# Kernel optimization log

Hardware: AMD Instinct MI355X
Metric: run time of the kernel (lower is better)

The kernel has to match this reference:

```python
import jax, jax.numpy as jnp
import numpy as np

K = 3  # == stride, neighbors per token


def setup_inputs() -> dict:
    key = jax.random.key(0)
    k1, k2, k3 = jax.random.split(key, 3)
    x = jax.random.normal(k1, (16, 64, 2048), dtype=jnp.float32)        # (B, C, T)
    W = jax.random.normal(k2, (64, 64, K), dtype=jnp.float32) * 0.05     # (O, I, K) conv1d weight
    b = jax.random.normal(k3, (64,), dtype=jnp.float32) * 0.05           # (O,) conv1d bias
    return {"x": x, "W": W, "b": b}


def reference(x, W, b):
    B, C, T = x.shape
    # pairwise squared euclidean distances over the channel dim: (B, T, T)
    nsq = jnp.sum(x * x, axis=1)                       # (B, T)
    dot = jnp.einsum('bct,bcs->bts', x, x)             # (B, T, T)
    dist = jnp.maximum(nsq[:, :, None] + nsq[:, None, :] - 2.0 * dot, 0.0)
    # K nearest neighbors (smallest distance -> top_k of negated dist)
    _, idx = jax.lax.top_k(-dist, K)                   # (B, T, K) int32 indices
    # gather neighbor features: prime[b, c, i*K + k] = x[b, c, idx[b, i, k]]
    idx_flat = idx.reshape(B, 1, T * K)
    prime = jnp.take_along_axis(x, jnp.broadcast_to(idx_flat, (B, C, T * K)), axis=2)
    # Conv1d with kernel_size=K, stride=K, padding=0 -> output length T
    out = jax.lax.conv_general_dilated(
        prime, W, window_strides=(K,), padding='VALID',
        dimension_numbers=('NCH', 'OIH', 'NCH'))
    return out + b[None, :, None]
```

## Files before the change

### kernel.cpp

```cpp
#include <hip/hip_runtime.h>

#define B_ 16
#define C_ 64
#define T_ 2048
#define O_ 64
#define KNN 3
#define HSPLIT 4
#define JCH (T_ / HSPLIT)
#define NJS (JCH / 32)

typedef short short8   __attribute__((ext_vector_type(8)));
typedef float f32x4    __attribute__((ext_vector_type(4)));
typedef unsigned short ushortx4 __attribute__((ext_vector_type(4)));

#define XT_OFF 0
#define XS_OFF (XT_OFF + B_ * T_ * C_)
#define NSQ_OFF (XS_OFF + B_ * T_ * C_)
#define WT_OFF (NSQ_OFF + B_ * T_)
#define CAND_OFF (WT_OFF + 192 * O_)

__device__ inline ushort bf16_rne(float f) {
    union { float f; unsigned u; } cv; cv.f = f;
    unsigned u = cv.u;
    u += 0x7FFF + ((u >> 16) & 1);
    return (ushort)(u >> 16);
}
__device__ inline float bf16_val(ushort h) {
    union { unsigned u; float f; } cv; cv.u = ((unsigned)h) << 16; return cv.f;
}

__global__ __launch_bounds__(256) void prep_kernel(const float* __restrict__ x,
                                                   const float* __restrict__ W,
                                                   float* __restrict__ ws) {
    float*  xT  = ws + XT_OFF;
    ushort* xs  = (ushort*)(ws + XS_OFF);
    float*  nsq = ws + NSQ_OFF;
    float*  Wt  = ws + WT_OFF;
    int blk = blockIdx.x;
    int tid = threadIdx.x;
    if (blk < B_ * (T_ / 64)) {
        int b  = blk / (T_ / 64);
        int t0 = (blk % (T_ / 64)) * 64;
        __shared__ float tl[64 * 65];
        #pragma unroll
        for (int r = 0; r < 4; ++r) {
            int c  = r * 16 + (tid >> 4);
            int t4 = (tid & 15) * 4;
            float4 v = *(const float4*)(x + (size_t)(b * C_ + c) * T_ + t0 + t4);
            tl[c * 65 + t4 + 0] = v.x;
            tl[c * 65 + t4 + 1] = v.y;
            tl[c * 65 + t4 + 2] = v.z;
            tl[c * 65 + t4 + 3] = v.w;
        }
        __syncthreads();
        #pragma unroll
        for (int r = 0; r < 4; ++r) {
            int t  = r * 16 + (tid >> 4);
            int c0 = (tid & 15) * 4;
            float v0 = tl[(c0 + 0) * 65 + t];
            float v1 = tl[(c0 + 1) * 65 + t];
            float v2 = tl[(c0 + 2) * 65 + t];
            float v3 = tl[(c0 + 3) * 65 + t];
            size_t rowg = (size_t)(b * T_ + t0 + t);
            float4 xv; xv.x = v0; xv.y = v1; xv.z = v2; xv.w = v3;
            *(float4*)(xT + rowg * 64 + c0) = xv;
            ushort h0 = bf16_rne(v0), h1 = bf16_rne(v1);
            ushort h2 = bf16_rne(v2), h3 = bf16_rne(v3);
            ushortx4 hv; hv[0] = h0; hv[1] = h1; hv[2] = h2; hv[3] = h3;
            ushortx4 lv;
            lv[0] = bf16_rne(v0 - bf16_val(h0));
            lv[1] = bf16_rne(v1 - bf16_val(h1));
            lv[2] = bf16_rne(v2 - bf16_val(h2));
            lv[3] = bf16_rne(v3 - bf16_val(h3));
            *(ushortx4*)(xs + rowg * 128 + c0)      = hv;
            *(ushortx4*)(xs + rowg * 128 + 64 + c0) = lv;
        }
        if (tid < 64) {
            float s = 0.f;
            #pragma unroll
            for (int c = 0; c < 64; ++c) { float v = tl[c * 65 + tid]; s = fmaf(v, v, s); }
            nsq[b * T_ + t0 + tid] = s;
        }
    } else {
        int e = (blk - B_ * (T_ / 64)) * 256 + tid;
        if (e < O_ * C_ * KNN) {
            int o = e / (C_ * KNN);
            int c = (e / KNN) % C_;
            int k = e % KNN;
            Wt[(k * 64 + c) * O_ + o] = W[e];
        }
    }
}

__global__ __launch_bounds__(256, 4) void knn_mfma_kernel(const ushort* __restrict__ xs,
                                                          const float* __restrict__ nsq,
                                                          ushort* __restrict__ cand) {
    __shared__ __align__(16) ushort jbuf[4][32 * 128];
    __shared__ float nsqs[JCH];

    int bid = blockIdx.x;
    int b   = (bid & 7) + 8 * (bid >> 9);
    int h   = (bid >> 3) & 3;
    int m   = (bid >> 5) & 15;
    int i0  = m * 128;
    int tid = threadIdx.x;
    int w   = tid >> 6, l = tid & 63, lr = l & 15, lq = l >> 4;
    const ushort* xsb = xs + (size_t)b * T_ * 128;
    int jBase = h * JCH;

    if (tid < JCH / 4)
        ((float4*)nsqs)[tid] = ((const float4*)(nsq + b * T_ + jBase))[tid];

    short8 bA0, bA1, bA4, bA5, bB0, bB1, bB4, bB5;
    {
        const ushort* ia = xsb + (size_t)(i0 + w * 32 + lr) * 128 + lq * 8;
        bA0 = *(const short8*)(ia + 0);  bA1 = *(const short8*)(ia + 32);
        bA4 = *(const short8*)(ia + 64); bA5 = *(const short8*)(ia + 96);
        const ushort* ib2 = ia + 16 * 128;
        bB0 = *(const short8*)(ib2 + 0);  bB1 = *(const short8*)(ib2 + 32);
        bB4 = *(const short8*)(ib2 + 64); bB5 = *(const short8*)(ib2 + 96);
    }
    float niA = nsq[b * T_ + i0 + w * 32 + lr] + 4.0f;
    float niB = nsq[b * T_ + i0 + w * 32 + 16 + lr] + 4.0f;

    const float INF = __builtin_inff();
    float kA0 = INF, kA1 = INF, kA2 = INF, kA3 = INF;
    float kB0 = INF, kB1 = INF, kB2 = INF, kB3 = INF;

    int cSw = lr ^ (w * 4 + lq);
    #define ISSUE_DMA(jsv, bufv) {                                               \
        _Pragma("unroll")                                                        \
        for (int p = 0; p < 2; ++p) {                                            \
            int rloc = p * 16 + w * 4 + lq;                                      \
            const ushort* gp = xsb + (size_t)(jBase + (jsv) * 32 + rloc) * 128 + cSw * 8; \
            __builtin_amdgcn_global_load_lds(                                    \
                (const __attribute__((address_space(1))) void*)gp,               \
                (__attribute__((address_space(3))) void*)(jbuf[bufv] + (p * 16 + w * 4) * 128), \
                16, 0, 0);                                                       \
        } }

    asm volatile("s_waitcnt lgkmcnt(0)" ::: "memory");

    ISSUE_DMA(0, 0);
    ISSUE_DMA(1, 1);
    ISSUE_DMA(2, 2);

    #pragma unroll 1
    for (int js = 0; js < NJS; ++js) {
        if (js <= NJS - 3)      asm volatile("s_waitcnt vmcnt(4)" ::: "memory");
        else if (js == NJS - 2) asm volatile("s_waitcnt vmcnt(2)" ::: "memory");
        else                    asm volatile("s_waitcnt vmcnt(0)" ::: "memory");
        __builtin_amdgcn_s_barrier();
        asm volatile("" ::: "memory");
        __builtin_amdgcn_sched_barrier(0);
        if (js + 3 < NJS) ISSUE_DMA(js + 3, (js + 3) & 3);
        const char* jb8 = (const char*)jbuf[js & 3];
        #pragma unroll
        for (int tile = 0; tile < 2; ++tile) {
            const char* rowp = jb8 + (tile * 16 + lr) * 256;
            short8 ah0 = *(const short8*)(rowp + ((( 0 + lq) ^ lr) << 4));
            short8 ah1 = *(const short8*)(rowp + ((( 4 + lq) ^ lr) << 4));
            short8 al0 = *(const short8*)(rowp + ((( 8 + lq) ^ lr) << 4));
            short8 al1 = *(const short8*)(rowp + (((12 + lq) ^ lr) << 4));
            f32x4 accA = {0.f, 0.f, 0.f, 0.f};
            f32x4 accB = {0.f, 0.f, 0.f, 0.f};
            accA = __builtin_amdgcn_mfma_f32_16x16x32_bf16(ah0, bA0, accA, 0, 0, 0);
            accB = __builtin_amdgcn_mfma_f32_16x16x32_bf16(ah0, bB0, accB, 0, 0, 0);
            accA = __builtin_amdgcn_mfma_f32_16x16x32_bf16(ah1, bA1, accA, 0, 0, 0);
            accB = __builtin_amdgcn_mfma_f32_16x16x32_bf16(ah1, bB1, accB, 0, 0, 0);
            accA = __builtin_amdgcn_mfma_f32_16x16x32_bf16(al0, bA0, accA, 0, 0, 0);
            accB = __builtin_amdgcn_mfma_f32_16x16x32_bf16(al0, bB0, accB, 0, 0, 0);
            accA = __builtin_amdgcn_mfma_f32_16x16x32_bf16(al1, bA1, accA, 0, 0, 0);
            accB = __builtin_amdgcn_mfma_f32_16x16x32_bf16(al1, bB1, accB, 0, 0, 0);
            accA = __builtin_amdgcn_mfma_f32_16x16x32_bf16(ah0, bA4, accA, 0, 0, 0);
            accB = __builtin_amdgcn_mfma_f32_16x16x32_bf16(ah0, bB4, accB, 0, 0, 0);
            accA = __builtin_amdgcn_mfma_f32_16x16x32_bf16(ah1, bA5, accA, 0, 0, 0);
            accB = __builtin_amdgcn_mfma_f32_16x16x32_bf16(ah1, bB5, accB, 0, 0, 0);
            float4 nv = *(const float4*)(nsqs + js * 32 + tile * 16 + lq * 4);
            int idb = ((js * 2 + tile) << 2) | (lq << 8);
            #define INS(K0, K1, K2, K3, sv, idv) {                                  \
                unsigned uu = (__float_as_uint(sv) & 0xFFFFFC00u) | (unsigned)(idv); \
                float kf = __uint_as_float(uu);                                      \
                float n0 = fminf(K0, kf);                                            \
                float n1 = __builtin_amdgcn_fmed3f(K0, K1, kf);                      \
                float n2 = __builtin_amdgcn_fmed3f(K1, K2, kf);                      \
                float n3 = __builtin_amdgcn_fmed3f(K2, K3, kf);                      \
                K0 = n0; K1 = n1; K2 = n2; K3 = n3; }
            {
                float s0 = fmaf(-2.f, accA[0], nv.x + niA); INS(kA0, kA1, kA2, kA3, s0, idb + 0);
                float s1 = fmaf(-2.f, accA[1], nv.y + niA); INS(kA0, kA1, kA2, kA3, s1, idb + 1);
                float s2 = fmaf(-2.f, accA[2], nv.z + niA); INS(kA0, kA1, kA2, kA3, s2, idb + 2);
                float s3 = fmaf(-2.f, accA[3], nv.w + niA); INS(kA0, kA1, kA2, kA3, s3, idb + 3);
            }
            {
                float s0 = fmaf(-2.f, accB[0], nv.x + niB); INS(kB0, kB1, kB2, kB3, s0, idb + 0);
                float s1 = fmaf(-2.f, accB[1], nv.y + niB); INS(kB0, kB1, kB2, kB3, s1, idb + 1);
                float s2 = fmaf(-2.f, accB[2], nv.z + niB); INS(kB0, kB1, kB2, kB3, s2, idb + 2);
                float s3 = fmaf(-2.f, accB[3], nv.w + niB); INS(kB0, kB1, kB2, kB3, s3, idb + 3);
            }
            #undef INS
        }
    }

    __syncthreads();
    float* fbuf = (float*)jbuf;
    {
        float* pa = fbuf + (w * 32 + lr) * 16 + lq * 4;
        pa[0] = kA0; pa[1] = kA1; pa[2] = kA2; pa[3] = kA3;
        float* pb = fbuf + (w * 32 + 16 + lr) * 16 + lq * 4;
        pb[0] = kB0; pb[1] = kB1; pb[2] = kB2; pb[3] = kB3;
    }
    __syncthreads();
    if (l < 32) {
        int rloc = w * 32 + l;
        const float* pr = fbuf + rloc * 16;
        float m0 = INF, m1 = INF, m2 = INF, m3 = INF;
        #pragma unroll
        for (int q2 = 0; q2 < 16; ++q2) {
            float kf = pr[q2];
            float n0 = fminf(m0, kf);
            float n1 = __builtin_amdgcn_fmed3f(m0, m1, kf);
            float n2 = __builtin_amdgcn_fmed3f(m1, m2, kf);
            float n3 = __builtin_amdgcn_fmed3f(m2, m3, kf);
            m0 = n0; m1 = n1; m2 = n2; m3 = n3;
        }
        ushortx4 cv;
        #define DEC(mf, slot) { unsigned u = __float_as_uint(mf) & 1023u;            \
            cv[slot] = (ushort)(jBase + (((u >> 2) & 63u) << 4) + ((u >> 8) << 2) + (u & 3)); }
        DEC(m0, 0); DEC(m1, 1); DEC(m2, 2); DEC(m3, 3);
        #undef DEC
        int row = b * T_ + i0 + rloc;
        *(ushortx4*)(cand + (size_t)row * 16 + h * 4) = cv;
    }
}

__global__ __launch_bounds__(256, 4) void conv_fused_kernel(const float* __restrict__ ws,
                                                            const float* __restrict__ bias,
                                                            float* __restrict__ out) {
    const float*  xT   = ws + XT_OFF;
    const float*  nsq  = ws + NSQ_OFF;
    const float*  Wt   = ws + WT_OFF;
    const ushort* cand = (const ushort*)(ws + CAND_OFF);

    __shared__ float g_s[192 * 32];
    __shared__ int   jsel3[32 * 3];

    float* sref = g_s;
    int*   jref = (int*)(g_s + 32 * 17);
    float* q_s  = g_s + 1152;

    int bid = blockIdx.x;
    int bb  = (bid & 7) + 8 * (bid >> 9);
    int i0  = ((bid >> 3) & 63) * 32;
    int tid = threadIdx.x;
    int w = tid >> 6, l = tid & 63;
    int bT = bb * T_;

    {
        int row = tid >> 3;
        int c8  = tid & 7;
        const float4* src = (const float4*)(xT + (size_t)(bT + i0 + row) * 64 + c8 * 8);
        float4 v0 = src[0], v1 = src[1];
        *(float4*)(q_s + row * 68 + c8 * 8)     = v0;
        *(float4*)(q_s + row * 68 + c8 * 8 + 4) = v1;
    }

    const float INF = __builtin_inff();
    int cd  = l >> 2;
    int c16 = l & 3;
    int rbase = i0 + w * 8;
    int jtA[8];
    #pragma unroll
    for (int rr = 0; rr < 8; ++rr)
        jtA[rr] = cand[(size_t)(bT + rbase + rr) * 16 + cd];
    float nsqj[8];
    #pragma unroll
    for (int rr = 0; rr < 8; ++rr)
        nsqj[rr] = nsq[bT + jtA[rr]];

    #pragma unroll
    for (int rp = 0; rp < 2; ++rp) {
        float4 bv0[4], bv1[4], bv2[4], bv3[4];
        #pragma unroll
        for (int r4 = 0; r4 < 4; ++r4) {
            const float4* bp = (const float4*)(xT + (size_t)(bT + jtA[rp * 4 + r4]) * 64 + c16 * 16);
            bv0[r4] = bp[0]; bv1[r4] = bp[1]; bv2[r4] = bp[2]; bv3[r4] = bp[3];
        }
        #pragma unroll
        for (int r4 = 0; r4 < 4; ++r4) {
            int rl = w * 8 + rp * 4 + r4;
            int jt = jtA[rp * 4 + r4];
            const float4* ap = (const float4*)(q_s + rl * 68 + c16 * 16);
            float4 a0 = ap[0], a1 = ap[1], a2 = ap[2], a3 = ap[3];
            float4 b0 = bv0[r4], b1 = bv1[r4], b2 = bv2[r4], b3 = bv3[r4];
            float p0 = fmaf(b0.w, a0.w, fmaf(b0.z, a0.z, fmaf(b0.y, a0.y, b0.x * a0.x)));
            float p1 = fmaf(b1.w, a1.w, fmaf(b1.z, a1.z, fmaf(b1.y, a1.y, b1.x * a1.x)));
            float p2 = fmaf(b2.w, a2.w, fmaf(b2.z, a2.z, fmaf(b2.y, a2.y, b2.x * a2.x)));
            float p3 = fmaf(b3.w, a3.w, fmaf(b3.z, a3.z, fmaf(b3.y, a3.y, b3.x * a3.x)));
            float p = (p0 + p1) + (p2 + p3);
            p += __shfl_xor(p, 1, 64);
            p += __shfl_xor(p, 2, 64);
            float s = nsqj[rp * 4 + r4] - 2.f * p;
            if (c16 == 0) { sref[rl * 17 + cd] = s; jref[rl * 17 + cd] = jt; }
        }
    }
    __syncthreads();

    if (tid < 32) {
        const float* sp = sref + tid * 17;
        const int*   jp = jref + tid * 17;
        float D0 = INF, D1 = INF, D2 = INF;
        int   I0 = 0x7FFFFFFF, I1 = 0x7FFFFFFF, I2 = 0x7FFFFFFF;
        #pragma unroll
        for (int t = 0; t < 16; ++t) {
            float s  = sp[t];
            int   jt = jp[t];
            bool lt2 = (s < D2) || (s == D2 && jt < I2);
            bool lt1 = (s < D1) || (s == D1 && jt < I1);
            bool lt0 = (s < D0) || (s == D0 && jt < I0);
            float nD2 = lt1 ? D1 : (lt2 ? s : D2); int nI2 = lt1 ? I1 : (lt2 ? jt : I2);
            float nD1 = lt0 ? D0 : (lt1 ? s : D1); int nI1 = lt0 ? I0 : (lt1 ? jt : I1);
            D2 = nD2; I2 = nI2; D1 = nD1; I1 = nI1;
            D0 = lt0 ? s : D0; I0 = lt0 ? jt : I0;
        }
        jsel3[tid * 3 + 0] = I0; jsel3[tid * 3 + 1] = I1; jsel3[tid * 3 + 2] = I2;
    }
    __syncthreads();

    if (tid < 192) {
        int k    = tid >> 6;
        int r6   = tid & 63;
        int ip   = r6 >> 1;
        int half = r6 & 1;
        int j = jsel3[ip * 3 + k];
        const float4* src = (const float4*)(xT + (size_t)(bT + j) * 64 + half * 32);
        #pragma unroll
        for (int q = 0; q < 8; ++q) {
            float4 v = src[q];
            int mm = k * 64 + (half * 8 + q) * 4;
            g_s[(mm + 0) * 32 + ip] = v.x;
            g_s[(mm + 1) * 32 + ip] = v.y;
            g_s[(mm + 2) * 32 + ip] = v.z;
            g_s[(mm + 3) * 32 + ip] = v.w;
        }
    }
    __syncthreads();

    int oq = tid >> 4;
    int iq = tid & 15;
    float a0x = 0.f, a0y = 0.f, a1x = 0.f, a1y = 0.f;
    float a2x = 0.f, a2y = 0.f, a3x = 0.f, a3y = 0.f;
    #pragma unroll 4
    for (int mm = 0; mm < 192; ++mm) {
        float4 wv = *(const float4*)(Wt + mm * 64 + oq * 4);
        float2 gv = *(const float2*)(g_s + mm * 32 + iq * 2);
        a0x = fmaf(wv.x, gv.x, a0x); a0y = fmaf(wv.x, gv.y, a0y);
        a1x = fmaf(wv.y, gv.x, a1x); a1y = fmaf(wv.y, gv.y, a1y);
        a2x = fmaf(wv.z, gv.x, a2x); a2y = fmaf(wv.z, gv.y, a2y);
        a3x = fmaf(wv.w, gv.x, a3x); a3y = fmaf(wv.w, gv.y, a3y);
    }
    int o0 = oq * 4;
    float b0 = bias[o0], b1 = bias[o0 + 1], b2 = bias[o0 + 2], b3 = bias[o0 + 3];
    float2 r0; r0.x = a0x + b0; r0.y = a0y + b0;
    float2 r1; r1.x = a1x + b1; r1.y = a1y + b1;
    float2 r2; r2.x = a2x + b2; r2.y = a2y + b2;
    float2 r3; r3.x = a3x + b3; r3.y = a3y + b3;
    size_t ob = (size_t)(bb * O_ + o0) * T_ + i0 + iq * 2;
    *(float2*)(out + ob)          = r0;
    *(float2*)(out + ob + T_)     = r1;
    *(float2*)(out + ob + 2 * T_) = r2;
    *(float2*)(out + ob + 3 * T_) = r3;
}

extern "C" void kernel_launch(void* const* d_in, const int* in_sizes, int n_in,
                              void* d_out, int out_size, void* d_ws, size_t ws_size,
                              hipStream_t stream) {
    const float* x    = (const float*)d_in[0];
    const float* W    = (const float*)d_in[1];
    const float* bias = (const float*)d_in[2];
    float* out = (float*)d_out;
    float* ws  = (float*)d_ws;

    prep_kernel<<<B_ * (T_ / 64) + 48, 256, 0, stream>>>(x, W, ws);
    knn_mfma_kernel<<<1024, 256, 0, stream>>>(
        (const ushort*)(ws + XS_OFF), ws + NSQ_OFF, (ushort*)(ws + CAND_OFF));
    conv_fused_kernel<<<B_ * 64, 256, 0, stream>>>(ws, bias, out);
}
```

Before: 136.3 us.

## Halve KNN query tile per block and use triple-buffered LDS for more occupancy

The KNN MFMA kernel now handles 64 query rows per block instead of 128, one 16-row tile per wave instead of two. It launches twice as many blocks, shrinks the LDS ring from four to three buffers with a two-ahead prefetch, and raises the launch-bounds occupancy hint. The aim is to cut per-block registers and LDS so more blocks fit per CU and latency hides better. In exchange, each staged key tile feeds half as many MFMAs, so global/LDS traffic per unit of compute doubles and the prefetch depth is shallower.

Measured after the change: 139.0 us. About the same (+2.0%).

```diff
diff --git a/kernel.cpp b/kernel.cpp
--- a/kernel.cpp
+++ b/kernel.cpp
@@ -92,17 +92,17 @@
     }
 }
 
-__global__ __launch_bounds__(256, 4) void knn_mfma_kernel(const ushort* __restrict__ xs,
+__global__ __launch_bounds__(256, 6) void knn_mfma_kernel(const ushort* __restrict__ xs,
                                                           const float* __restrict__ nsq,
                                                           ushort* __restrict__ cand) {
-    __shared__ __align__(16) ushort jbuf[4][32 * 128];
+    __shared__ __align__(16) ushort jbuf[3][32 * 128];
     __shared__ float nsqs[JCH];
 
     int bid = blockIdx.x;
-    int b   = (bid & 7) + 8 * (bid >> 9);
+    int b   = (bid & 7) + 8 * (bid >> 10);
     int h   = (bid >> 3) & 3;
-    int m   = (bid >> 5) & 15;
-    int i0  = m * 128;
+    int m   = (bid >> 5) & 31;
+    int i0  = m * 64;
     int tid = threadIdx.x;
     int w   = tid >> 6, l = tid & 63, lr = l & 15, lq = l >> 4;
     const ushort* xsb = xs + (size_t)b * T_ * 128;
@@ -111,21 +111,16 @@
     if (tid < JCH / 4)
         ((float4*)nsqs)[tid] = ((const float4*)(nsq + b * T_ + jBase))[tid];
 
-    short8 bA0, bA1, bA4, bA5, bB0, bB1, bB4, bB5;
+    short8 bA0, bA1, bA4, bA5;
     {
-        const ushort* ia = xsb + (size_t)(i0 + w * 32 + lr) * 128 + lq * 8;
+        const ushort* ia = xsb + (size_t)(i0 + w * 16 + lr) * 128 + lq * 8;
         bA0 = *(const short8*)(ia + 0);  bA1 = *(const short8*)(ia + 32);
         bA4 = *(const short8*)(ia + 64); bA5 = *(const short8*)(ia + 96);
-        const ushort* ib2 = ia + 16 * 128;
-        bB0 = *(const short8*)(ib2 + 0);  bB1 = *(const short8*)(ib2 + 32);
-        bB4 = *(const short8*)(ib2 + 64); bB5 = *(const short8*)(ib2 + 96);
-    }
-    float niA = nsq[b * T_ + i0 + w * 32 + lr] + 4.0f;
-    float niB = nsq[b * T_ + i0 + w * 32 + 16 + lr] + 4.0f;
+    }
+    float niA = nsq[b * T_ + i0 + w * 16 + lr] + 4.0f;
 
     const float INF = __builtin_inff();
     float kA0 = INF, kA1 = INF, kA2 = INF, kA3 = INF;
-    float kB0 = INF, kB1 = INF, kB2 = INF, kB3 = INF;
 
     int cSw = lr ^ (w * 4 + lq);
     #define ISSUE_DMA(jsv, bufv) {                                               \
@@ -143,18 +138,16 @@
 
     ISSUE_DMA(0, 0);
     ISSUE_DMA(1, 1);
-    ISSUE_DMA(2, 2);
 
     #pragma unroll 1
     for (int js = 0; js < NJS; ++js) {
-        if (js <= NJS - 3)      asm volatile("s_waitcnt vmcnt(4)" ::: "memory");
-        else if (js == NJS - 2) asm volatile("s_waitcnt vmcnt(2)" ::: "memory");
-        else                    asm volatile("s_waitcnt vmcnt(0)" ::: "memory");
+        if (js < NJS - 1) asm volatile("s_waitcnt vmcnt(2)" ::: "memory");
+        else              asm volatile("s_waitcnt vmcnt(0)" ::: "memory");
         __builtin_amdgcn_s_barrier();
         asm volatile("" ::: "memory");
         __builtin_amdgcn_sched_barrier(0);
-        if (js + 3 < NJS) ISSUE_DMA(js + 3, (js + 3) & 3);
-        const char* jb8 = (const char*)jbuf[js & 3];
+        if (js + 2 < NJS) ISSUE_DMA(js + 2, (js + 2) % 3);
+        const char* jb8 = (const char*)jbuf[js % 3];
         #pragma unroll
         for (int tile = 0; tile < 2; ++tile) {
             const char* rowp = jb8 + (tile * 16 + lr) * 256;
@@ -163,19 +156,12 @@
             short8 al0 = *(const short8*)(rowp + ((( 8 + lq) ^ lr) << 4));
             short8 al1 = *(const short8*)(rowp + (((12 + lq) ^ lr) << 4));
             f32x4 accA = {0.f, 0.f, 0.f, 0.f};
-            f32x4 accB = {0.f, 0.f, 0.f, 0.f};
             accA = __builtin_amdgcn_mfma_f32_16x16x32_bf16(ah0, bA0, accA, 0, 0, 0);
-            accB = __builtin_amdgcn_mfma_f32_16x16x32_bf16(ah0, bB0, accB, 0, 0, 0);
             accA = __builtin_amdgcn_mfma_f32_16x16x32_bf16(ah1, bA1, accA, 0, 0, 0);
-            accB = __builtin_amdgcn_mfma_f32_16x16x32_bf16(ah1, bB1, accB, 0, 0, 0);
             accA = __builtin_amdgcn_mfma_f32_16x16x32_bf16(al0, bA0, accA, 0, 0, 0);
-            accB = __builtin_amdgcn_mfma_f32_16x16x32_bf16(al0, bB0, accB, 0, 0, 0);
             accA = __builtin_amdgcn_mfma_f32_16x16x32_bf16(al1, bA1, accA, 0, 0, 0);
-            accB = __builtin_amdgcn_mfma_f32_16x16x32_bf16(al1, bB1, accB, 0, 0, 0);
             accA = __builtin_amdgcn_mfma_f32_16x16x32_bf16(ah0, bA4, accA, 0, 0, 0);
-            accB = __builtin_amdgcn_mfma_f32_16x16x32_bf16(ah0, bB4, accB, 0, 0, 0);
             accA = __builtin_amdgcn_mfma_f32_16x16x32_bf16(ah1, bA5, accA, 0, 0, 0);
-            accB = __builtin_amdgcn_mfma_f32_16x16x32_bf16(ah1, bB5, accB, 0, 0, 0);
             float4 nv = *(const float4*)(nsqs + js * 32 + tile * 16 + lq * 4);
             int idb = ((js * 2 + tile) << 2) | (lq << 8);
             #define INS(K0, K1, K2, K3, sv, idv) {                                  \
@@ -192,12 +178,6 @@
                 float s2 = fmaf(-2.f, accA[2], nv.z + niA); INS(kA0, kA1, kA2, kA3, s2, idb + 2);
                 float s3 = fmaf(-2.f, accA[3], nv.w + niA); INS(kA0, kA1, kA2, kA3, s3, idb + 3);
             }
-            {
-                float s0 = fmaf(-2.f, accB[0], nv.x + niB); INS(kB0, kB1, kB2, kB3, s0, idb + 0);
-                float s1 = fmaf(-2.f, accB[1], nv.y + niB); INS(kB0, kB1, kB2, kB3, s1, idb + 1);
-                float s2 = fmaf(-2.f, accB[2], nv.z + niB); INS(kB0, kB1, kB2, kB3, s2, idb + 2);
-                float s3 = fmaf(-2.f, accB[3], nv.w + niB); INS(kB0, kB1, kB2, kB3, s3, idb + 3);
-            }
             #undef INS
         }
     }
@@ -205,15 +185,12 @@
     __syncthreads();
     float* fbuf = (float*)jbuf;
     {
-        float* pa = fbuf + (w * 32 + lr) * 16 + lq * 4;
+        float* pa = fbuf + (w * 16 + lr) * 16 + lq * 4;
         pa[0] = kA0; pa[1] = kA1; pa[2] = kA2; pa[3] = kA3;
-        float* pb = fbuf + (w * 32 + 16 + lr) * 16 + lq * 4;
-        pb[0] = kB0; pb[1] = kB1; pb[2] = kB2; pb[3] = kB3;
-    }
-    __syncthreads();
-    if (l < 32) {
-        int rloc = w * 32 + l;
-        const float* pr = fbuf + rloc * 16;
+    }
+    __syncthreads();
+    if (tid < 64) {
+        const float* pr = fbuf + tid * 16;
         float m0 = INF, m1 = INF, m2 = INF, m3 = INF;
         #pragma unroll
         for (int q2 = 0; q2 < 16; ++q2) {
@@ -229,7 +206,7 @@
             cv[slot] = (ushort)(jBase + (((u >> 2) & 63u) << 4) + ((u >> 8) << 2) + (u & 3)); }
         DEC(m0, 0); DEC(m1, 1); DEC(m2, 2); DEC(m3, 3);
         #undef DEC
-        int row = b * T_ + i0 + rloc;
+        int row = b * T_ + i0 + tid;
         *(ushortx4*)(cand + (size_t)row * 16 + h * 4) = cv;
     }
 }
@@ -382,7 +359,7 @@
     float* ws  = (float*)d_ws;
 
     prep_kernel<<<B_ * (T_ / 64) + 48, 256, 0, stream>>>(x, W, ws);
-    knn_mfma_kernel<<<1024, 256, 0, stream>>>(
+    knn_mfma_kernel<<<2048, 256, 0, stream>>>(
         (const ushort*)(ws + XS_OFF), ws + NSQ_OFF, (ushort*)(ws + CAND_OFF));
     conv_fused_kernel<<<B_ * 64, 256, 0, stream>>>(ws, bias, out);
 }
```
